# Performance work log

Hardware: AMD Instinct MI355X
Metric: run time of the kernel (lower is better)

The kernel has to match this reference:

```python
import jax, jax.numpy as jnp
import numpy as np

BATCH, SEQ, HIDDEN, HEAD, VDIM = 4, 4096, 256, 64, 64
GAMMA = 0.96875
SCALE_BASE = 512.0


def _xpos(x, downscale):
    # x: [B, L, d] ; standard RetNet XPOS (rotary + exponential position scale)
    L, d = x.shape[1], x.shape[2]
    half = d // 2
    pos = jnp.arange(L, dtype=jnp.float32)
    scale_vec = (jnp.arange(0, d, 2, dtype=jnp.float32) + 0.4 * d) / (1.4 * d)  # [d/2]
    scale = scale_vec[None, :] ** (pos[:, None] / SCALE_BASE)                   # [L, d/2]
    inv_freq = 1.0 / (10000.0 ** (jnp.arange(half, dtype=jnp.float32) / half))  # [d/2]
    sinusoid = pos[:, None] * inv_freq[None, :]                                 # [L, d/2]
    sin, cos = jnp.sin(sinusoid), jnp.cos(sinusoid)
    if downscale:
        scale = 1.0 / scale
    sin2 = jnp.repeat(sin * scale, 2, axis=-1)  # duplicate_interleave -> [L, d]
    cos2 = jnp.repeat(cos * scale, 2, axis=-1)
    x1, x2 = x[..., ::2], x[..., 1::2]
    rot = jnp.stack((-x2, x1), axis=-1).reshape(x.shape)  # rotate_every_two
    return x * cos2[None] + rot * sin2[None]


def setup_inputs() -> dict:
    key = jax.random.key(0)
    k1, k2, k3, k4 = jax.random.split(key, 4)
    X = jax.random.normal(k1, (BATCH, SEQ, HIDDEN), dtype=jnp.float32)
    W_Q = jax.random.normal(k2, (HIDDEN, HEAD), dtype=jnp.float32) / HIDDEN
    W_K = jax.random.normal(k3, (HIDDEN, HEAD), dtype=jnp.float32) / HIDDEN
    W_V = jax.random.normal(k4, (HIDDEN, VDIM), dtype=jnp.float32) / HIDDEN
    return {"X": X, "W_Q": W_Q, "W_K": W_K, "W_V": W_V}


def reference(X, W_Q, W_K, W_V):
    Q = _xpos(X @ W_Q, downscale=False)   # [B, L, d]
    K = _xpos(X @ W_K, downscale=True)    # [B, L, d]
    V = X @ W_V                           # [B, L, v]
    L = X.shape[1]
    n = jnp.arange(L)
    diff = n[:, None] - n[None, :]
    # D[n, m] = gamma^(n-m) for n >= m, else 0 (NaN/overflow-safe via clamped exponent)
    D = jnp.where(diff >= 0,
                  GAMMA ** jnp.where(diff >= 0, diff, 0).astype(jnp.float32),
                  0.0)
    scores = jnp.einsum('bnd,bmd->bnm', Q, K) * D[None]  # [B, L, L]
    return scores @ V                                     # [B, L, v]
```

## Files before the change

### kernel.cpp

```cpp
#include <hip/hip_runtime.h>
#include <hip/hip_bf16.h>
#include <math.h>


#define SEQ    4096
#define NB     4
#define HID    256
#define HD     64
#define WT     3

typedef short          bf16x8 __attribute__((ext_vector_type(8)));
typedef float          f32x4  __attribute__((ext_vector_type(4)));
typedef unsigned short u16;
typedef unsigned int   u32;
typedef u16            u16x8  __attribute__((ext_vector_type(8)));
typedef u16            u16x4  __attribute__((ext_vector_type(4)));

__device__ __forceinline__ u16 f2bf(float f) {
    __hip_bfloat16 h = __float2bfloat16(f);
    return __builtin_bit_cast(u16, h);
}

__global__ __launch_bounds__(256)
void prep_kernel(const float* __restrict__ WQ, const float* __restrict__ WK,
                 const float* __restrict__ WV, float* __restrict__ Tbl,
                 u16* __restrict__ Wf)
{
    const int t = threadIdx.x;
    if (blockIdx.x < 512) {
        const int p = blockIdx.x * 256 + t;
        const int n = p >> 5, i = p & 31;
        const float sv = (2.f * (float)i + 25.6f) / 89.6f;
        const float sc = powf(sv, (float)n * (1.f / 512.f));
        const float inv_freq = 1.f / powf(10000.f, (float)i * (1.f / 32.f));
        float sn, cs;
        sincosf((float)n * inv_freq, &sn, &cs);
        float4 o;
        o.x = cs * sc; o.y = sn * sc;
        o.z = cs / sc; o.w = sn / sc;
        reinterpret_cast<float4*>(Tbl)[p] = o;
    } else {
        const int p = (blockIdx.x - 512) * 256 + t;
        const int lane = p & 63;
        const int kc   = (p >> 6) & 7;
        const int ct   = p >> 9;
        const int col  = ct * 16 + (lane & 15);
        const float* Wsrc = (col < 64) ? WQ : (col < 128) ? WK : WV;
        const int c = col & 63;
        u16x8 hv;
#pragma unroll
        for (int j = 0; j < 8; ++j)
            hv[j] = f2bf(Wsrc[(kc * 32 + (lane >> 4) * 8 + j) * HD + c]);
        *reinterpret_cast<u16x8*>(&Wf[(size_t)p * 8]) = hv;
    }
}

#define XLDS 264

__global__ __launch_bounds__(1024, 4)
void proj_kernel(const float* __restrict__ X, const float* __restrict__ Tbl,
                 const u16* __restrict__ Wf,
                 u16* __restrict__ Qb, u16* __restrict__ Kb, u16* __restrict__ Vb)
{
    __shared__ __align__(16) u16 Xhs[64 * XLDS];
    const int t = threadIdx.x;
    const int row0 = blockIdx.x * 64;

    for (int e = t; e < 64 * 64; e += 1024) {
        const int r = e >> 6, k4 = (e & 63) << 2;
        const float4 xv = *reinterpret_cast<const float4*>(&X[(size_t)(row0 + r) * HID + k4]);
        u16x4 hv;
#pragma unroll
        for (int j = 0; j < 4; ++j) hv[j] = f2bf((&xv.x)[j]);
        *reinterpret_cast<u16x4*>(&Xhs[r * XLDS + k4]) = hv;
    }
    __syncthreads();

    const int lane = t & 63;
    const int w    = t >> 6;
    const int rt   = w >> 2;
    const int ch   = w & 3;
    const int frow = rt * 16 + (lane & 15);
    const int fk   = (lane >> 4) * 8;

    f32x4 acc[3];
#pragma unroll
    for (int i = 0; i < 3; ++i) acc[i] = (f32x4)0.f;

#pragma unroll
    for (int kc = 0; kc < 8; ++kc) {
        const bf16x8 ah = *reinterpret_cast<const bf16x8*>(&Xhs[frow * XLDS + kc * 32 + fk]);
#pragma unroll
        for (int ctp = 0; ctp < 3; ++ctp) {
            const int ct = ch * 3 + ctp;
            const size_t fb = (size_t)((ct * 8 + kc) * 64 + lane) * 8;
            const bf16x8 wh = *reinterpret_cast<const bf16x8*>(&Wf[fb]);
            acc[ctp] = __builtin_amdgcn_mfma_f32_16x16x32_bf16(ah, wh, acc[ctp], 0, 0, 0);
        }
    }

    const int sel   = lane & 1;
    const int c16   = lane & 15;
    const int rbase = (lane >> 4) * 4;

#pragma unroll
    for (int ctp = 0; ctp < 3; ++ctp) {
        const int ct = ch * 3 + ctp;
        float xp[4];
#pragma unroll
        for (int reg = 0; reg < 4; ++reg)
            xp[reg] = __shfl_xor(acc[ctp][reg], 1, 64);
#pragma unroll
        for (int rr = 0; rr < 2; ++rr) {
            const int reg = sel * 2 + rr;
            const float xe = sel ? xp[reg] : acc[ctp][reg];
            const float xo = sel ? acc[ctp][reg] : xp[reg];
            const int r = row0 + rt * 16 + rbase + reg;
            if (ct < 8) {
                const bool isK = ct >= 4;
                const int cq0 = (ct & 3) * 16 + (c16 & ~1);
                const int i   = cq0 >> 1;
                const int n   = r & (SEQ - 1);
                const float4 tb = reinterpret_cast<const float4*>(Tbl)[n * 32 + i];
                const float cs = isK ? tb.z : tb.x;
                const float sn = isK ? tb.w : tb.y;
                const float oe = xe * cs - xo * sn;
                const float oo = xo * cs + xe * sn;
                const u32 hw = (u32)f2bf(oe) | ((u32)f2bf(oo) << 16);
                u32* P = reinterpret_cast<u32*>(isK ? Kb : Qb);
                P[(r * HD + cq0) >> 1] = hw;
            } else {
                const int cv0 = (ct - 8) * 16 + (c16 & ~1);
                const u32 w32 = (u32)f2bf(xe) | ((u32)f2bf(xo) << 16);
                reinterpret_cast<u32*>(Vb)[(r * HD + cv0) >> 1] = w32;
            }
        }
    }
}

#define KRS 72
#define SW  72

__global__ __launch_bounds__(1024, 4)
void retention_kernel(const u16* __restrict__ Qb, const u16* __restrict__ Kb,
                      const u16* __restrict__ Vb, float* __restrict__ Out)
{
    __shared__ __align__(16) u16 Khs[2][64 * KRS];
    __shared__ __align__(16) u16 Vts[3][64 * KRS];
    __shared__ __align__(16) u16 Ss [2][64 * SW];

    const int t    = threadIdx.x;
    const int lane = t & 63;
    const int w    = t >> 6;
    const int rb   = w >> 2;
    const int cb   = w & 3;

    const int flat = blockIdx.x + 64 * blockIdx.y;
    const int work = (flat & 7) * 32 + (flat >> 3);
    const int nt   = work & 63;
    const int b    = work >> 6;
    const int n0   = nt * 64;
    const int bbase = b * SEQ;

    const int half = t >> 9;
    const int th   = t & 511;
    const int srow = th >> 3;
    const int scol = (th & 7) * 8;
    const int vch  = ((srow >> 3) ^ (th & 7)) & 7;
    const int vidx = vch * 8 + (srow & 7);

    const int mt0 = (nt >= WT) ? (nt - WT) : 0;

    {
        const int gk = (bbase + mt0 * 64 + srow) * HD + scol;
        if (half == 0) {
            *reinterpret_cast<u16x8*>(&Khs[0][srow * KRS + scol]) =
                *reinterpret_cast<const u16x8*>(&Kb[gk]);
        } else {
            const u16x8 vv = *reinterpret_cast<const u16x8*>(&Vb[gk]);
#pragma unroll
            for (int j = 0; j < 8; ++j)
                Vts[0][(scol + j) * KRS + vidx] = vv[j];
        }
    }

    const int frow = rb * 16 + (lane & 15);
    const int fk   = (lane >> 4) * 8;
    const size_t gq = (size_t)(bbase + n0 + frow) * HD + fk;
    const bf16x8 qb0 = *reinterpret_cast<const bf16x8*>(&Qb[gq]);
    const bf16x8 qb1 = *reinterpret_cast<const bf16x8*>(&Qb[gq + 32]);
    __syncthreads();

    const float log2g = -0.04580368544f;
    const int nlocB = rb * 16 + (lane >> 4) * 4;
    const int mloc  = cb * 16 + (lane & 15);
    float gd[4]; int dd[4];
#pragma unroll
    for (int reg = 0; reg < 4; ++reg) {
        dd[reg] = nlocB + reg - mloc;
        gd[reg] = exp2f((float)dd[reg] * log2g);
    }

    f32x4 accO = (f32x4)0.f;
    const int mrow = cb * 16 + (lane & 15);
    const int c0 = ((lane >> 4)     ^ (mrow >> 3)) & 7;
    const int c1 = (((lane >> 4) + 4) ^ (mrow >> 3)) & 7;

    int curV = 0;
    for (int mt = mt0, i = 0; mt <= nt; ++mt, ++i) {
        const int cur  = i & 1;
        const int m0   = mt * 64;
        const bool pref = (mt < nt);
        const int wV   = (curV == 2) ? 0 : curV + 1;

        u16x8 pk, pv;
        if (pref) {
            const int gk = (bbase + m0 + 64 + srow) * HD + scol;
            if (half == 0) pk = *reinterpret_cast<const u16x8*>(&Kb[gk]);
            else           pv = *reinterpret_cast<const u16x8*>(&Vb[gk]);
        }

        const bf16x8 kb0 = *reinterpret_cast<const bf16x8*>(&Khs[cur][mrow * KRS + fk]);
        const bf16x8 kb1 = *reinterpret_cast<const bf16x8*>(&Khs[cur][mrow * KRS + 32 + fk]);
        f32x4 accS = (f32x4)0.f;
        accS = __builtin_amdgcn_mfma_f32_16x16x32_bf16(qb0, kb0, accS, 0, 0, 0);
        accS = __builtin_amdgcn_mfma_f32_16x16x32_bf16(qb1, kb1, accS, 0, 0, 0);

        const float gs = exp2f((float)(n0 - m0) * log2g);
#pragma unroll
        for (int reg = 0; reg < 4; ++reg) {
            const int d   = (n0 - m0) + dd[reg];
            const float g = (d >= 0) ? gs * gd[reg] : 0.f;
            Ss[cur][(nlocB + reg) * SW + mloc] = f2bf(accS[reg] * g);
        }

        if (pref) {
            if (half == 0) {
                *reinterpret_cast<u16x8*>(&Khs[cur ^ 1][srow * KRS + scol]) = pk;
            } else {
#pragma unroll
                for (int j = 0; j < 8; ++j)
                    Vts[wV][(scol + j) * KRS + vidx] = pv[j];
            }
        }

        __syncthreads();

        const bf16x8 s0 = *reinterpret_cast<const bf16x8*>(&Ss[cur][frow * SW + fk]);
        const bf16x8 s1 = *reinterpret_cast<const bf16x8*>(&Ss[cur][frow * SW + 32 + fk]);
        const bf16x8 v0 = *reinterpret_cast<const bf16x8*>(&Vts[curV][mrow * KRS + c0 * 8]);
        const bf16x8 v1 = *reinterpret_cast<const bf16x8*>(&Vts[curV][mrow * KRS + c1 * 8]);
        accO = __builtin_amdgcn_mfma_f32_16x16x32_bf16(s0, v0, accO, 0, 0, 0);
        accO = __builtin_amdgcn_mfma_f32_16x16x32_bf16(s1, v1, accO, 0, 0, 0);

        curV = wV;
    }

    const int v = cb * 16 + (lane & 15);
#pragma unroll
    for (int reg = 0; reg < 4; ++reg) {
        const int n = n0 + rb * 16 + (lane >> 4) * 4 + reg;
        Out[(size_t)(bbase + n) * HD + v] = accO[reg];
    }
}

extern "C" void kernel_launch(void* const* d_in, const int* in_sizes, int n_in,
                              void* d_out, int out_size, void* d_ws, size_t ws_size,
                              hipStream_t stream)
{
    const float* X  = (const float*)d_in[0];
    const float* WQ = (const float*)d_in[1];
    const float* WK = (const float*)d_in[2];
    const float* WV = (const float*)d_in[3];
    float* Out = (float*)d_out;

    char* ws = (char*)d_ws;
    const size_t SZ = (size_t)NB * SEQ * HD * sizeof(u16);
    u16* Qb = (u16*)(ws);
    u16* Kb = (u16*)(ws + SZ);
    u16* Vb = (u16*)(ws + 2 * SZ);
    float* Tbl = (float*)(ws + 3 * SZ);
    u16* Wf = (u16*)(ws + 4 * SZ);

    prep_kernel<<<dim3(536), 256, 0, stream>>>(WQ, WK, WV, Tbl, Wf);
    proj_kernel<<<dim3(256), 1024, 0, stream>>>(
        X, Tbl, Wf, Qb, Kb, Vb);
    retention_kernel<<<dim3(64, NB), 1024, 0, stream>>>(
        Qb, Kb, Vb, Out);
}
```

Measured before the change: 27.27 us.

## Preload whole K/V window into LDS and compute scores per-wave without barriers

The kernel now loads all K and V tiles of the decay window into shared memory up front, with a single barrier, instead of double-buffering tile by tile with a barrier every iteration. Each wave computes the full 16x64 score block it needs (four MFMA pairs) into a private LDS scratch area, so no cross-wave exchange of scores is required. This removes the per-tile __syncthreads and the prefetch logic. In exchange, each wave redoes QK^T work that its sibling waves also compute (4x redundant score MFMAs), uses more LDS for the whole window, and no longer overlaps loads with compute.

```diff
diff --git a/kernel.cpp b/kernel.cpp
--- a/kernel.cpp
+++ b/kernel.cpp
@@ -139,15 +139,15 @@
 }
 
 #define KRS 72
-#define SW  72
+#define TL  (64 * KRS)
 
 __global__ __launch_bounds__(1024, 4)
 void retention_kernel(const u16* __restrict__ Qb, const u16* __restrict__ Kb,
                       const u16* __restrict__ Vb, float* __restrict__ Out)
 {
-    __shared__ __align__(16) u16 Khs[2][64 * KRS];
-    __shared__ __align__(16) u16 Vts[3][64 * KRS];
-    __shared__ __align__(16) u16 Ss [2][64 * SW];
+    __shared__ __align__(16) u16 Khs[(WT + 1) * TL];
+    __shared__ __align__(16) u16 Vts[(WT + 1) * TL];
+    __shared__ __align__(16) u16 Sw [16][16 * KRS];
 
     const int t    = threadIdx.x;
     const int lane = t & 63;
@@ -162,105 +162,92 @@
     const int n0   = nt * 64;
     const int bbase = b * SEQ;
 
-    const int half = t >> 9;
-    const int th   = t & 511;
-    const int srow = th >> 3;
-    const int scol = (th & 7) * 8;
-    const int vch  = ((srow >> 3) ^ (th & 7)) & 7;
-    const int vidx = vch * 8 + (srow & 7);
-
     const int mt0 = (nt >= WT) ? (nt - WT) : 0;
-
-    {
-        const int gk = (bbase + mt0 * 64 + srow) * HD + scol;
-        if (half == 0) {
-            *reinterpret_cast<u16x8*>(&Khs[0][srow * KRS + scol]) =
-                *reinterpret_cast<const u16x8*>(&Kb[gk]);
-        } else {
-            const u16x8 vv = *reinterpret_cast<const u16x8*>(&Vb[gk]);
-#pragma unroll
-            for (int j = 0; j < 8; ++j)
-                Vts[0][(scol + j) * KRS + vidx] = vv[j];
-        }
-    }
-
-    const int frow = rb * 16 + (lane & 15);
+    const int nts = nt - mt0 + 1;
+
+    for (int s = t; s < nts * 512; s += 1024) {
+        const int ti    = s >> 9;
+        const int sl    = s & 511;
+        const int row   = sl >> 3;
+        const int chunk = sl & 7;
+        const size_t g  = (size_t)(bbase + (mt0 + ti) * 64 + row) * HD + chunk * 8;
+        *reinterpret_cast<u16x8*>(&Khs[ti * TL + row * KRS + chunk * 8]) =
+            *reinterpret_cast<const u16x8*>(&Kb[g]);
+        const u16x8 vv = *reinterpret_cast<const u16x8*>(&Vb[g]);
+        const int vidx = ((((row >> 3) ^ chunk) & 7) << 3) + (row & 7);
+#pragma unroll
+        for (int j = 0; j < 8; ++j)
+            Vts[ti * TL + (chunk * 8 + j) * KRS + vidx] = vv[j];
+    }
+
     const int fk   = (lane >> 4) * 8;
-    const size_t gq = (size_t)(bbase + n0 + frow) * HD + fk;
+    const int qrow = rb * 16 + (lane & 15);
+    const size_t gq = (size_t)(bbase + n0 + qrow) * HD + fk;
     const bf16x8 qb0 = *reinterpret_cast<const bf16x8*>(&Qb[gq]);
     const bf16x8 qb1 = *reinterpret_cast<const bf16x8*>(&Qb[gq + 32]);
-    __syncthreads();
 
     const float log2g = -0.04580368544f;
     const int nlocB = rb * 16 + (lane >> 4) * 4;
-    const int mloc  = cb * 16 + (lane & 15);
-    float gd[4]; int dd[4];
+    int   ddc[4];
+    float gdm[4][4];
 #pragma unroll
     for (int reg = 0; reg < 4; ++reg) {
-        dd[reg] = nlocB + reg - mloc;
-        gd[reg] = exp2f((float)dd[reg] * log2g);
-    }
+        ddc[reg] = nlocB + reg - (lane & 15);
+#pragma unroll
+        for (int mti = 0; mti < 4; ++mti)
+            gdm[mti][reg] = exp2f((float)(ddc[reg] - 16 * mti) * log2g);
+    }
+
+    u16* const sS = &Sw[w][0];
+    const int nl16 = lane & 15;
+    const int vrow = cb * 16 + nl16;
+    const int c0 = ((lane >> 4)     ^ (vrow >> 3)) & 7;
+    const int c1 = (((lane >> 4) + 4) ^ (vrow >> 3)) & 7;
 
     f32x4 accO = (f32x4)0.f;
-    const int mrow = cb * 16 + (lane & 15);
-    const int c0 = ((lane >> 4)     ^ (mrow >> 3)) & 7;
-    const int c1 = (((lane >> 4) + 4) ^ (mrow >> 3)) & 7;
-
-    int curV = 0;
-    for (int mt = mt0, i = 0; mt <= nt; ++mt, ++i) {
-        const int cur  = i & 1;
-        const int m0   = mt * 64;
-        const bool pref = (mt < nt);
-        const int wV   = (curV == 2) ? 0 : curV + 1;
-
-        u16x8 pk, pv;
-        if (pref) {
-            const int gk = (bbase + m0 + 64 + srow) * HD + scol;
-            if (half == 0) pk = *reinterpret_cast<const u16x8*>(&Kb[gk]);
-            else           pv = *reinterpret_cast<const u16x8*>(&Vb[gk]);
-        }
-
-        const bf16x8 kb0 = *reinterpret_cast<const bf16x8*>(&Khs[cur][mrow * KRS + fk]);
-        const bf16x8 kb1 = *reinterpret_cast<const bf16x8*>(&Khs[cur][mrow * KRS + 32 + fk]);
-        f32x4 accS = (f32x4)0.f;
-        accS = __builtin_amdgcn_mfma_f32_16x16x32_bf16(qb0, kb0, accS, 0, 0, 0);
-        accS = __builtin_amdgcn_mfma_f32_16x16x32_bf16(qb1, kb1, accS, 0, 0, 0);
+
+    __syncthreads();
+
+    for (int ti = 0; ti < nts; ++ti) {
+        const int m0 = (mt0 + ti) * 64;
+        const u16* Kt = &Khs[ti * TL];
+        const u16* Vt = &Vts[ti * TL];
+
+        f32x4 accS[4];
+#pragma unroll
+        for (int mti = 0; mti < 4; ++mti) {
+            const bf16x8 kb0 = *reinterpret_cast<const bf16x8*>(&Kt[(mti * 16 + nl16) * KRS + fk]);
+            const bf16x8 kb1 = *reinterpret_cast<const bf16x8*>(&Kt[(mti * 16 + nl16) * KRS + 32 + fk]);
+            f32x4 a = (f32x4)0.f;
+            a = __builtin_amdgcn_mfma_f32_16x16x32_bf16(qb0, kb0, a, 0, 0, 0);
+            a = __builtin_amdgcn_mfma_f32_16x16x32_bf16(qb1, kb1, a, 0, 0, 0);
+            accS[mti] = a;
+        }
 
         const float gs = exp2f((float)(n0 - m0) * log2g);
 #pragma unroll
-        for (int reg = 0; reg < 4; ++reg) {
-            const int d   = (n0 - m0) + dd[reg];
-            const float g = (d >= 0) ? gs * gd[reg] : 0.f;
-            Ss[cur][(nlocB + reg) * SW + mloc] = f2bf(accS[reg] * g);
-        }
-
-        if (pref) {
-            if (half == 0) {
-                *reinterpret_cast<u16x8*>(&Khs[cur ^ 1][srow * KRS + scol]) = pk;
-            } else {
-#pragma unroll
-                for (int j = 0; j < 8; ++j)
-                    Vts[wV][(scol + j) * KRS + vidx] = pv[j];
+        for (int mti = 0; mti < 4; ++mti) {
+#pragma unroll
+            for (int reg = 0; reg < 4; ++reg) {
+                const int d   = (n0 - m0) + ddc[reg] - 16 * mti;
+                const float g = (d >= 0) ? gs * gdm[mti][reg] : 0.f;
+                sS[((lane >> 4) * 4 + reg) * KRS + mti * 16 + nl16] =
+                    f2bf(accS[mti][reg] * g);
             }
         }
 
-        __syncthreads();
-
-        const bf16x8 s0 = *reinterpret_cast<const bf16x8*>(&Ss[cur][frow * SW + fk]);
-        const bf16x8 s1 = *reinterpret_cast<const bf16x8*>(&Ss[cur][frow * SW + 32 + fk]);
-        const bf16x8 v0 = *reinterpret_cast<const bf16x8*>(&Vts[curV][mrow * KRS + c0 * 8]);
-        const bf16x8 v1 = *reinterpret_cast<const bf16x8*>(&Vts[curV][mrow * KRS + c1 * 8]);
+        const bf16x8 s0 = *reinterpret_cast<const bf16x8*>(&sS[nl16 * KRS + fk]);
+        const bf16x8 s1 = *reinterpret_cast<const bf16x8*>(&sS[nl16 * KRS + 32 + fk]);
+        const bf16x8 v0 = *reinterpret_cast<const bf16x8*>(&Vt[vrow * KRS + c0 * 8]);
+        const bf16x8 v1 = *reinterpret_cast<const bf16x8*>(&Vt[vrow * KRS + c1 * 8]);
         accO = __builtin_amdgcn_mfma_f32_16x16x32_bf16(s0, v0, accO, 0, 0, 0);
         accO = __builtin_amdgcn_mfma_f32_16x16x32_bf16(s1, v1, accO, 0, 0, 0);
-
-        curV = wV;
-    }
-
-    const int v = cb * 16 + (lane & 15);
+    }
+
 #pragma unroll
     for (int reg = 0; reg < 4; ++reg) {
-        const int n = n0 + rb * 16 + (lane >> 4) * 4 + reg;
-        Out[(size_t)(bbase + n) * HD + v] = accO[reg];
+        const int n = n0 + nlocB + reg;
+        Out[(size_t)(bbase + n) * HD + cb * 16 + nl16] = accO[reg];
     }
 }
 
```

Measured after the change: 29.75 us. +9.1%, slower.
